# Optimization experiments

Hardware: AMD Instinct MI355X
Metric: run time of the kernel (lower is better)

## Reference

```python
import jax, jax.numpy as jnp
import numpy as np

NINPUTS = 16
WIDTH = 128
KSIZE = 21
SPP = 8
BS, CI, H, W = 2, 3, 192, 192
EPS = 1e-08


def _conv(x, w, b, padding):
    y = jax.lax.conv_general_dilated(
        x, w, window_strides=(1, 1), padding=padding,
        dimension_numbers=("NCHW", "OIHW", "NCHW"))
    return y + b[None, :, None, None]


def apply_kernels(kernel, radiance, ksize):
    """Per-pixel predicted-kernel conv: fused gather-multiply-reduce over taps.
    kernel: (bs, ksize^2, kh, kw), radiance: (bs, ci, h, w).
    Replicates torch apply_kernels (normalization='sum') without materializing
    the (bs, ci, kh, kw, ksize^2) unfold tile tensor."""
    bs, k2, kh, kw = kernel.shape
    _, ci, h, w = radiance.shape
    needed = kh + ksize - 1
    if needed > h:
        crop = (needed - h) // 2
        if crop > 0:
            kernel = kernel[:, :, crop:-crop, crop:-crop]
        kh, kw = kernel.shape[2], kernel.shape[3]
    else:
        crop = (h - needed) // 2
        if crop > 0:
            radiance = radiance[:, :, crop:-crop, crop:-crop]
    taps = jnp.arange(k2, dtype=jnp.int32)
    dy = taps // ksize
    dx = taps % ksize

    def body(acc, idx):
        patch = jax.lax.dynamic_slice(radiance, (0, 0, dy[idx], dx[idx]),
                                      (bs, ci, kh, kw))
        kv = jax.lax.dynamic_slice_in_dim(kernel, idx, 1, axis=1)  # (bs,1,kh,kw)
        return acc + kv * patch, None

    acc0 = jnp.zeros((bs, ci, kh, kw), radiance.dtype)
    weighted_sum, _ = jax.lax.scan(body, acc0, taps)
    kernel_sum = jnp.sum(kernel, axis=1, keepdims=True)  # (bs,1,kh,kw)
    return weighted_sum, kernel_sum


def setup_inputs() -> dict:
    key = jax.random.key(0)
    ks = jax.random.split(key, 10)
    s = 0.05
    inp = {
        "features": jax.random.normal(ks[0], (BS, SPP, NINPUTS, H, W), jnp.float32),
        "radiance": jax.random.uniform(ks[1], (BS, SPP, CI, H, W), jnp.float32),
        # recurrent conv processor (simplified main_processor): SAME 3x3 conv
        "w_rnn": jax.random.normal(ks[2], (WIDTH, NINPUTS + WIDTH, 3, 3), jnp.float32) * s,
        "b_rnn": jnp.zeros((WIDTH,), jnp.float32),
        "w_k1": jax.random.normal(ks[3], (WIDTH, WIDTH + NINPUTS, 3, 3), jnp.float32) * s,
        "b_k1": jnp.zeros((WIDTH,), jnp.float32),
        "w_k2": jax.random.normal(ks[4], (WIDTH, WIDTH, 3, 3), jnp.float32) * s,
        "b_k2": jnp.zeros((WIDTH,), jnp.float32),
        "w_k3": jax.random.normal(ks[5], (KSIZE * KSIZE, WIDTH, 3, 3), jnp.float32) * s,
        "b_k3": jnp.zeros((KSIZE * KSIZE,), jnp.float32),
    }
    return inp


def reference(features, radiance, w_rnn, b_rnn, w_k1, b_k1, w_k2, b_k2, w_k3, b_k3):
    bs, spp, ci, h, w = radiance.shape
    lrelu = lambda x: jax.nn.leaky_relu(x, 0.01)
    state = jnp.zeros((bs, WIDTH, h, w), features.dtype)
    unnorm = sumw = max_k = None
    for step in range(spp):
        f = features[:, step]  # (bs, ninputs, h, w)
        rnn = lrelu(_conv(jnp.concatenate([f, state], axis=1), w_rnn, b_rnn, "SAME"))
        state = rnn
        nf = jnp.concatenate([rnn, f], axis=1)  # (bs, width+ninputs, h, w)
        k = lrelu(_conv(nf, w_k1, b_k1, "VALID"))
        k = lrelu(_conv(k, w_k2, b_k2, "VALID"))
        k = _conv(k, w_k3, b_k3, "VALID")  # (bs, ksize^2, h-6, w-6), linear out
        # online-softmax (flash-attention-style) running max/exp rescale
        new_max = jnp.max(k.reshape(bs, -1), axis=1).reshape(bs, 1, 1, 1)
        if step == 0:
            max_k = new_max
        else:
            old_max = max_k
            max_k = jnp.maximum(old_max, new_max)
        kern = jnp.exp(k - max_k)
        ws, ksum = apply_kernels(kern, radiance[:, step], KSIZE)
        if step == 0:
            unnorm, sumw = ws, ksum
        else:
            scale = jnp.exp(old_max - max_k)
            unnorm = unnorm * scale + ws
            sumw = sumw * scale + ksum
    return unnorm / (sumw + EPS)
```

## Files before the change

kernel.cpp:

```cpp
#include <hip/hip_runtime.h>
#include <stdint.h>

typedef _Float16 half8 __attribute__((ext_vector_type(8)));
typedef _Float16 half4 __attribute__((ext_vector_type(4)));
typedef __attribute__((ext_vector_type(8))) short short8;
typedef __attribute__((ext_vector_type(4))) float f32x4;

__device__ __forceinline__ unsigned encf(float x){
  uint32_t u = __float_as_uint(x);
  return (u & 0x80000000u) ? ~u : (u | 0x80000000u);
}
__device__ __forceinline__ float decf(unsigned u){
  uint32_t b = (u & 0x80000000u) ? (u & 0x7FFFFFFFu) : ~u;
  return __uint_as_float(b);
}
__device__ __forceinline__ void gload16(const void* g, void* l){
  __builtin_amdgcn_global_load_lds(
      (const __attribute__((address_space(1))) void*)g,
      (__attribute__((address_space(3))) void*)l, 16, 0, 0);
}

__global__ __launch_bounds__(256) void zero_u32(unsigned* __restrict__ p, int n){
  for (int i = blockIdx.x*256 + threadIdx.x; i < n; i += gridDim.x*256) p[i] = 0u;
}

__global__ __launch_bounds__(256) void pack_w(const float* __restrict__ w, _Float16* __restrict__ wp,
                                              int CO, int CI, int COP, int CINP){
  int idx = blockIdx.x*256 + threadIdx.x;
  int total = 9*COP*CINP;
  if (idx >= total) return;
  int ci = idx % CINP;
  int rest = idx / CINP;
  int co = rest % COP;
  int t  = rest / COP;
  float v = 0.f;
  if (co < CO && ci < CI) v = w[((size_t)co*CI + ci)*9 + t];
  int kc = ci >> 5, cr = ci & 31;
  wp[(((size_t)kc*9 + t)*COP + co)*32 + cr] = (_Float16)v;
}

__global__ __launch_bounds__(256) void pack_bias(const float* __restrict__ b, float* __restrict__ bp, int n, int npad){
  int i = blockIdx.x*256 + threadIdx.x;
  if (i < npad) bp[i] = (i < n) ? b[i] : 0.f;
}

__global__ __launch_bounds__(256) void pack_feat(const float* __restrict__ f,
                                                 _Float16* __restrict__ rnn_in,
                                                 _Float16* __restrict__ k1_in,
                                                 int copy_state,
                                                 unsigned fbstr, unsigned rbstr, unsigned kbstr){
  int p = blockIdx.x*256 + threadIdx.x;
  if (p >= 36864) return;
  int b = blockIdx.y;
  int y = p / 192, x = p % 192;
  const float* fb = f + (size_t)b*fbstr;
  _Float16* r = rnn_in + (size_t)b*rbstr + ((size_t)(y+1)*194 + (x+1))*160;
  _Float16* k = k1_in  + (size_t)b*kbstr + (size_t)p*160;
  #pragma unroll
  for (int c = 0; c < 16; ++c){
    _Float16 v = (_Float16)fb[c*36864 + p];
    r[c] = v;
    k[128 + c] = v;
  }
  if (copy_state){
    #pragma unroll
    for (int cc = 0; cc < 128; cc += 8)
      *reinterpret_cast<short8*>(r + 16 + cc) = *reinterpret_cast<const short8*>(k + cc);
  }
}

template<int CINP, bool RELU, bool K3>
__global__ __launch_bounds__(256, 3) void conv3(
    const _Float16* __restrict__ X, int Wst, unsigned xbstr,
    const _Float16* __restrict__ Wp, int COP,
    const float* __restrict__ bias,
    _Float16* __restrict__ Y, int Wst_out, int DCP, unsigned ybstr,
    unsigned* __restrict__ slot, int Ho, int Wo,
    int nco_mask, int nco_shift)
{
  constexpr int KC = CINP/32;
  __shared__ _Float16 lds[2][6528];

  const int tid  = threadIdx.x;
  const int lane = tid & 63;
  const int wid  = tid >> 6;
  const int wm   = wid & 1;
  const int wq   = wid >> 1;
  const int l15  = lane & 15, lg = lane >> 4;
  const int xb   = blockIdx.x * 32;
  const int yb   = blockIdx.y * 4;
  const int co_blk = blockIdx.z & nco_mask;
  const int b      = blockIdx.z >> nco_shift;
  const int co_base = co_blk * 128;

  const _Float16* Xb = X + (size_t)b * xbstr;

  uint32_t goff[4];
  #pragma unroll
  for (int k = 0; k < 4; ++k){
    int item = k*256 + tid;
    int col = item % 34;
    int q   = item / 34;
    int sg  = q & 3;
    int row = q >> 2;
    int pix = (yb + row)*Wst + xb + col;
    goff[k] = (uint32_t)(((uint32_t)pix*CINP + sg*8) * 2);
  }

  auto stage = [&](int buf, int kc){
    const char* xp = (const char*)Xb + (size_t)kc*64;
    char* lb = (char*)&lds[buf][0];
    #pragma unroll
    for (int k = 0; k < 3; ++k)
      gload16(xp + goff[k], lb + k*4096 + wid*1024);
    if (tid < 48)
      gload16(xp + goff[3], lb + 3*4096 + wid*1024);
  };

  uint32_t boffe[4];
  #pragma unroll
  for (int n = 0; n < 4; ++n)
    boffe[n] = (uint32_t)((((wq*2 + (n>>1))*4 + lg)*34 + (n&1)*16 + l15) * 8);

  f32x4 acc[4][4] = {};
  const _Float16* wlane = Wp + ((size_t)(co_base + wm*64 + l15)*32 + lg*8);
  const size_t wtap = (size_t)COP*32;

  stage(0, 0);
  __syncthreads();
  for (int kc = 0; kc < KC; ++kc){
    if (kc + 1 < KC) stage((kc+1)&1, kc+1);
    const _Float16* wt = wlane + (size_t)kc*9*wtap;
    const _Float16* lb = &lds[kc&1][0];
    half8 wreg[2][4], breg[2][4];
    #pragma unroll
    for (int i = 0; i < 4; ++i)
      wreg[0][i] = *reinterpret_cast<const half8*>(wt + (size_t)i*512);
    #pragma unroll
    for (int n = 0; n < 4; ++n)
      breg[0][n] = *reinterpret_cast<const half8*>(lb + boffe[n]);
    #pragma unroll
    for (int t = 0; t < 9; ++t){
      const int cur = t & 1, nxt = cur ^ 1;
      if (t < 8){
        const int ky = (t+1)/3, kx = (t+1) - ky*3;
        const _Float16* wn = wt + (size_t)(t+1)*wtap;
        #pragma unroll
        for (int i = 0; i < 4; ++i)
          wreg[nxt][i] = *reinterpret_cast<const half8*>(wn + (size_t)i*512);
        #pragma unroll
        for (int n = 0; n < 4; ++n)
          breg[nxt][n] = *reinterpret_cast<const half8*>(lb + boffe[n] + (ky*136 + kx)*8);
      }
      #pragma unroll
      for (int n = 0; n < 4; ++n)
        #pragma unroll
        for (int i = 0; i < 4; ++i)
          acc[i][n] = __builtin_amdgcn_mfma_f32_16x16x32_f16(wreg[cur][i], breg[cur][n], acc[i][n], 0, 0, 0);
      __builtin_amdgcn_sched_group_barrier(0x020, 4, 0);
      __builtin_amdgcn_sched_group_barrier(0x100, 4, 0);
      __builtin_amdgcn_sched_group_barrier(0x008, 16, 0);
    }
    if (kc + 1 < KC) __syncthreads();
  }

  float lmax = -3.0e38f;
  #pragma unroll
  for (int i = 0; i < 4; ++i){
    const int cb = co_base + wm*64 + i*16 + lg*4;
    f32x4 bs = *reinterpret_cast<const f32x4*>(bias + cb);
    #pragma unroll
    for (int n = 0; n < 4; ++n){
      const int y = yb + wq*2 + (n>>1);
      const int x = xb + (n&1)*16 + l15;
      if (y < Ho && x < Wo){
        float v[4];
        #pragma unroll
        for (int j = 0; j < 4; ++j){
          float t = acc[i][n][j] + bs[j];
          if (RELU) t = t > 0.f ? t : 0.01f*t;
          v[j] = t;
        }
        if constexpr (!K3){
          half4 pk;
          #pragma unroll
          for (int j = 0; j < 4; ++j) pk[j] = (_Float16)v[j];
          *reinterpret_cast<half4*>(Y + (size_t)b*ybstr + ((size_t)y*Wst_out + x)*DCP + cb) = pk;
        } else {
          _Float16* yp = Y + (size_t)b*ybstr;
          #pragma unroll
          for (int j = 0; j < 4; ++j){
            if (cb + j < 441){
              yp[(size_t)(cb+j)*34596 + (size_t)y*186 + x] = (_Float16)v[j];
              lmax = fmaxf(lmax, v[j]);
            }
          }
        }
      }
    }
  }
  if constexpr (K3){
    #pragma unroll
    for (int o = 32; o > 0; o >>= 1) lmax = fmaxf(lmax, __shfl_xor(lmax, o));
    if (lane == 0) atomicMax(slot + b, encf(lmax));
  }
}

__global__ void update_max(float* __restrict__ st, unsigned* __restrict__ slot, int step){
  int b = threadIdx.x;
  if (b < 2){
    float nm   = decf(slot[b]);
    float oldM = st[2*b];
    float M    = (step == 0) ? nm : fmaxf(oldM, nm);
    st[2*b+1] = (step == 0) ? 0.f : expf(oldM - M);
    st[2*b]   = M;
    slot[b] = 0u;
  }
}

__global__ __launch_bounds__(256) void apply_acc(
    const _Float16* __restrict__ k3out, const float* __restrict__ rad,
    const float* __restrict__ st,
    float* __restrict__ unnorm, float* __restrict__ sumw)
{
  const int tx = threadIdx.x & 63, ty = threadIdx.x >> 6;
  const int x = blockIdx.x*64 + tx;
  const int y = blockIdx.y*4 + ty;
  const int b = blockIdx.z;
  if (x >= 172 || y >= 172) return;
  const float M = st[2*b], scale = st[2*b+1];
  const _Float16* kp = k3out + (size_t)b*15256836 + (size_t)(y+7)*186 + (x+7);
  const float* rb = rad + (size_t)b*884736;
  float a0 = 0.f, a1 = 0.f, a2 = 0.f, aw = 0.f;
  for (int dy = 0; dy < 21; ++dy){
    const float* r0 = rb + (size_t)(y+dy)*192 + x;
    #pragma unroll
    for (int dx = 0; dx < 21; ++dx){
      float w = __expf((float)kp[(size_t)(dy*21+dx)*34596] - M);
      aw += w;
      a0 += w * r0[dx];
      a1 += w * r0[36864 + dx];
      a2 += w * r0[73728 + dx];
    }
  }
  size_t p = (size_t)b*88752 + (size_t)y*172 + x;
  size_t ps = (size_t)b*29584 + (size_t)y*172 + x;
  unnorm[p]        = unnorm[p]*scale        + a0;
  unnorm[p+29584]  = unnorm[p+29584]*scale  + a1;
  unnorm[p+59168]  = unnorm[p+59168]*scale  + a2;
  sumw[ps]         = sumw[ps]*scale         + aw;
}

__global__ __launch_bounds__(256) void finalize_out(const float* __restrict__ unnorm,
                                                    const float* __restrict__ sumw,
                                                    float* __restrict__ out){
  int i = blockIdx.x*256 + threadIdx.x;
  int b = blockIdx.y;
  if (i >= 88752) return;
  int p = i % 29584;
  out[(size_t)b*88752 + i] = unnorm[(size_t)b*88752 + i] / (sumw[(size_t)b*29584 + p] + 1e-8f);
}

extern "C" void kernel_launch(void* const* d_in, const int* in_sizes, int n_in,
                              void* d_out, int out_size, void* d_ws, size_t ws_size,
                              hipStream_t stream) {
  const float* features = (const float*)d_in[0];
  const float* radiance = (const float*)d_in[1];
  const float* w_rnn = (const float*)d_in[2];
  const float* b_rnn = (const float*)d_in[3];
  const float* w_k1  = (const float*)d_in[4];
  const float* b_k1  = (const float*)d_in[5];
  const float* w_k2  = (const float*)d_in[6];
  const float* b_k2  = (const float*)d_in[7];
  const float* w_k3  = (const float*)d_in[8];
  const float* b_k3  = (const float*)d_in[9];
  float* out = (float*)d_out;

  char* ws = (char*)d_ws;
  size_t off = 0;
  auto alloc = [&](size_t bytes)->char*{
    char* p = ws + off;
    off = (off + bytes + 255) & ~(size_t)255;
    return p;
  };
  _Float16* wp_rnn   = (_Float16*)alloc((size_t)9*128*160*2);
  _Float16* wp_k1    = (_Float16*)alloc((size_t)9*128*160*2);
  _Float16* wp_k2    = (_Float16*)alloc((size_t)9*128*128*2);
  _Float16* wp_k3    = (_Float16*)alloc((size_t)9*512*128*2);
  float*    bias_k3p = (float*)   alloc((size_t)512*4);
  const unsigned RB = 194u*194u*160u;
  const unsigned KB = (192u*192u+448u)*160u;
  const unsigned K2B = (190u*190u+444u)*128u;
  const unsigned K3B = (188u*188u+440u)*128u;
  const unsigned KOB = 441u*34596u;
  _Float16* rnn_in = (_Float16*)alloc((size_t)2*RB*2);
  _Float16* k1_in  = (_Float16*)alloc((size_t)2*KB*2);
  _Float16* k2_in  = (_Float16*)alloc((size_t)2*K2B*2);
  _Float16* k3_in  = (_Float16*)alloc((size_t)2*K3B*2);
  _Float16* k3_out = (_Float16*)alloc((size_t)2*KOB*2);
  float*    accz   = (float*)   alloc((size_t)236678*4);
  if (off > ws_size) return;

  float*    unnorm = accz;
  float*    sumw   = accz + 177504;
  float*    st     = accz + 236672;
  unsigned* slot   = (unsigned*)(accz + 236676);

  pack_w<<<(9*128*160+255)/256, 256, 0, stream>>>(w_rnn, wp_rnn, 128, 144, 128, 160);
  pack_w<<<(9*128*160+255)/256, 256, 0, stream>>>(w_k1,  wp_k1,  128, 144, 128, 160);
  pack_w<<<(9*128*128+255)/256, 256, 0, stream>>>(w_k2,  wp_k2,  128, 128, 128, 128);
  pack_w<<<(9*512*128+255)/256, 256, 0, stream>>>(w_k3,  wp_k3,  441, 128, 512, 128);
  pack_bias<<<2, 256, 0, stream>>>(b_k3, bias_k3p, 441, 512);

  zero_u32<<<2048, 256, 0, stream>>>((unsigned*)rnn_in, (int)(2*RB/2));
  zero_u32<<<925,  256, 0, stream>>>((unsigned*)accz, 236678);

  for (int s = 0; s < 8; ++s){
    const float* f   = features + (size_t)s*16*36864;
    const float* rad = radiance + (size_t)s*3*36864;
    pack_feat<<<dim3(144,2), 256, 0, stream>>>(f, rnn_in, k1_in, s > 0 ? 1 : 0,
                                               8u*16u*36864u, RB, KB);
    conv3<160,true ,false><<<dim3(6,48,2), 256, 0, stream>>>(
        rnn_in, 194, RB, wp_rnn, 128, b_rnn, k1_in, 192, 160, KB,
        nullptr, 192, 192, 0, 0);
    conv3<160,true ,false><<<dim3(6,48,2), 256, 0, stream>>>(
        k1_in, 192, KB, wp_k1, 128, b_k1, k2_in, 190, 128, K2B,
        nullptr, 190, 190, 0, 0);
    conv3<128,true ,false><<<dim3(6,47,2), 256, 0, stream>>>(
        k2_in, 190, K2B, wp_k2, 128, b_k2, k3_in, 188, 128, K3B,
        nullptr, 188, 188, 0, 0);
    conv3<128,false,true ><<<dim3(6,47,8), 256, 0, stream>>>(
        k3_in, 188, K3B, wp_k3, 512, bias_k3p, k3_out, 0, 0, KOB,
        slot, 186, 186, 3, 2);
    update_max<<<1, 64, 0, stream>>>(st, slot, s);
    apply_acc<<<dim3(3,43,2), 256, 0, stream>>>(k3_out, rad, st, unnorm, sumw);
  }
  finalize_out<<<dim3(347,2), 256, 0, stream>>>(unnorm, sumw, out);
}
```

Measured before the change: 2.743 ms.

## Halve row tile for first three convs and raise occupancy target

Templates the conv kernel on the number of output rows per block. The three 128-channel convs now use 2-row tiles with twice as many blocks, and the K3 conv keeps 4 rows. Launch bounds go from 3 to 6 waves per SIMD, and the manual MFMA/load schedule-group barriers are removed. The intent is more resident blocks and better load balance across CUs, which hides latency better. The cost is more halo reloads per output (4 staged rows for 2 outputs) and less weight reuse per block. The higher occupancy target may also cause register spills in the 4-row variant.

After: 6.807 ms. 2.48x slower.

```diff
diff --git a/kernel.cpp b/kernel.cpp
--- a/kernel.cpp
+++ b/kernel.cpp
@@ -69,8 +69,8 @@
   }
 }
 
-template<int CINP, bool RELU, bool K3>
-__global__ __launch_bounds__(256, 3) void conv3(
+template<int CINP, int NROW, bool RELU, bool K3>
+__global__ __launch_bounds__(256, 6) void conv3(
     const _Float16* __restrict__ X, int Wst, unsigned xbstr,
     const _Float16* __restrict__ Wp, int COP,
     const float* __restrict__ bias,
@@ -79,7 +79,11 @@
     int nco_mask, int nco_shift)
 {
   constexpr int KC = CINP/32;
-  __shared__ _Float16 lds[2][6528];
+  constexpr int RPW = NROW/2;
+  constexpr int SROWS = NROW + 2;
+  constexpr int ITEMS = SROWS*4*34;
+  constexpr int NRND  = (ITEMS + 255)/256;
+  __shared__ _Float16 lds[2][ITEMS*8];
 
   const int tid  = threadIdx.x;
   const int lane = tid & 63;
@@ -88,41 +92,46 @@
   const int wq   = wid >> 1;
   const int l15  = lane & 15, lg = lane >> 4;
   const int xb   = blockIdx.x * 32;
-  const int yb   = blockIdx.y * 4;
+  const int yb   = blockIdx.y * NROW;
   const int co_blk = blockIdx.z & nco_mask;
   const int b      = blockIdx.z >> nco_shift;
   const int co_base = co_blk * 128;
 
   const _Float16* Xb = X + (size_t)b * xbstr;
 
-  uint32_t goff[4];
+  uint32_t goff[NRND];
   #pragma unroll
-  for (int k = 0; k < 4; ++k){
+  for (int k = 0; k < NRND; ++k){
     int item = k*256 + tid;
-    int col = item % 34;
-    int q   = item / 34;
-    int sg  = q & 3;
-    int row = q >> 2;
-    int pix = (yb + row)*Wst + xb + col;
-    goff[k] = (uint32_t)(((uint32_t)pix*CINP + sg*8) * 2);
+    if (item < ITEMS){
+      int col = item % 34;
+      int q   = item / 34;
+      int sg  = q & 3;
+      int row = q >> 2;
+      int pix = (yb + row)*Wst + xb + col;
+      goff[k] = (uint32_t)(((uint32_t)pix*CINP + sg*8) * 2);
+    } else goff[k] = 0;
   }
 
   auto stage = [&](int buf, int kc){
     const char* xp = (const char*)Xb + (size_t)kc*64;
     char* lb = (char*)&lds[buf][0];
     #pragma unroll
-    for (int k = 0; k < 3; ++k)
-      gload16(xp + goff[k], lb + k*4096 + wid*1024);
-    if (tid < 48)
-      gload16(xp + goff[3], lb + 3*4096 + wid*1024);
+    for (int k = 0; k < NRND; ++k){
+      if (k*256 + tid < ITEMS)
+        gload16(xp + goff[k], lb + k*4096 + wid*1024);
+    }
   };
 
-  uint32_t boffe[4];
+  uint32_t boffe[NROW];
   #pragma unroll
-  for (int n = 0; n < 4; ++n)
-    boffe[n] = (uint32_t)((((wq*2 + (n>>1))*4 + lg)*34 + (n&1)*16 + l15) * 8);
-
-  f32x4 acc[4][4] = {};
+  for (int n = 0; n < NROW; ++n){
+    int nR = (NROW == 4) ? (n >> 1) : 0;
+    int nC = (NROW == 4) ? (n & 1)  : n;
+    boffe[n] = (uint32_t)((((wq*RPW + nR)*4 + lg)*34 + nC*16 + l15) * 8);
+  }
+
+  f32x4 acc[4][NROW] = {};
   const _Float16* wlane = Wp + ((size_t)(co_base + wm*64 + l15)*32 + lg*8);
   const size_t wtap = (size_t)COP*32;
 
@@ -132,12 +141,12 @@
     if (kc + 1 < KC) stage((kc+1)&1, kc+1);
     const _Float16* wt = wlane + (size_t)kc*9*wtap;
     const _Float16* lb = &lds[kc&1][0];
-    half8 wreg[2][4], breg[2][4];
+    half8 wreg[2][4], breg[2][NROW];
     #pragma unroll
     for (int i = 0; i < 4; ++i)
       wreg[0][i] = *reinterpret_cast<const half8*>(wt + (size_t)i*512);
     #pragma unroll
-    for (int n = 0; n < 4; ++n)
+    for (int n = 0; n < NROW; ++n)
       breg[0][n] = *reinterpret_cast<const half8*>(lb + boffe[n]);
     #pragma unroll
     for (int t = 0; t < 9; ++t){
@@ -149,17 +158,14 @@
         for (int i = 0; i < 4; ++i)
           wreg[nxt][i] = *reinterpret_cast<const half8*>(wn + (size_t)i*512);
         #pragma unroll
-        for (int n = 0; n < 4; ++n)
+        for (int n = 0; n < NROW; ++n)
           breg[nxt][n] = *reinterpret_cast<const half8*>(lb + boffe[n] + (ky*136 + kx)*8);
       }
       #pragma unroll
-      for (int n = 0; n < 4; ++n)
+      for (int n = 0; n < NROW; ++n)
         #pragma unroll
         for (int i = 0; i < 4; ++i)
           acc[i][n] = __builtin_amdgcn_mfma_f32_16x16x32_f16(wreg[cur][i], breg[cur][n], acc[i][n], 0, 0, 0);
-      __builtin_amdgcn_sched_group_barrier(0x020, 4, 0);
-      __builtin_amdgcn_sched_group_barrier(0x100, 4, 0);
-      __builtin_amdgcn_sched_group_barrier(0x008, 16, 0);
     }
     if (kc + 1 < KC) __syncthreads();
   }
@@ -170,9 +176,11 @@
     const int cb = co_base + wm*64 + i*16 + lg*4;
     f32x4 bs = *reinterpret_cast<const f32x4*>(bias + cb);
     #pragma unroll
-    for (int n = 0; n < 4; ++n){
-      const int y = yb + wq*2 + (n>>1);
-      const int x = xb + (n&1)*16 + l15;
+    for (int n = 0; n < NROW; ++n){
+      const int nR = (NROW == 4) ? (n >> 1) : 0;
+      const int nC = (NROW == 4) ? (n & 1)  : n;
+      const int y = yb + wq*RPW + nR;
+      const int x = xb + nC*16 + l15;
       if (y < Ho && x < Wo){
         float v[4];
         #pragma unroll
@@ -320,16 +328,16 @@
     const float* rad = radiance + (size_t)s*3*36864;
     pack_feat<<<dim3(144,2), 256, 0, stream>>>(f, rnn_in, k1_in, s > 0 ? 1 : 0,
                                                8u*16u*36864u, RB, KB);
-    conv3<160,true ,false><<<dim3(6,48,2), 256, 0, stream>>>(
+    conv3<160,2,true ,false><<<dim3(6,96,2), 256, 0, stream>>>(
         rnn_in, 194, RB, wp_rnn, 128, b_rnn, k1_in, 192, 160, KB,
         nullptr, 192, 192, 0, 0);
-    conv3<160,true ,false><<<dim3(6,48,2), 256, 0, stream>>>(
+    conv3<160,2,true ,false><<<dim3(6,95,2), 256, 0, stream>>>(
         k1_in, 192, KB, wp_k1, 128, b_k1, k2_in, 190, 128, K2B,
         nullptr, 190, 190, 0, 0);
-    conv3<128,true ,false><<<dim3(6,47,2), 256, 0, stream>>>(
+    conv3<128,2,true ,false><<<dim3(6,94,2), 256, 0, stream>>>(
         k2_in, 190, K2B, wp_k2, 128, b_k2, k3_in, 188, 128, K3B,
         nullptr, 188, 188, 0, 0);
-    conv3<128,false,true ><<<dim3(6,47,8), 256, 0, stream>>>(
+    conv3<128,4,false,true ><<<dim3(6,47,8), 256, 0, stream>>>(
         k3_in, 188, K3B, wp_k3, 512, bias_k3p, k3_out, 0, 0, KOB,
         slot, 186, 186, 3, 2);
     update_max<<<1, 64, 0, stream>>>(st, slot, s);
```
